# Performance work log

Measured on AMD Instinct MI355X. Metric: run time of the kernel, lower is better.

The kernel has to match this reference:

```python
import jax, jax.numpy as jnp
import numpy as np

DIM = 2048
N_HEADS = 16
HEAD_DIM = DIM // N_HEADS
GROUP_SIZE = 128
THRESHOLD = 0.5
EPS = 1e-8
B, T = 2, 2048


def _ternary_dequant(w):
    # groupwise absmean ternary quantize + dequant; DIM % GROUP_SIZE == 0 so no pad
    O, I = w.shape
    g = I // GROUP_SIZE
    wg = w.reshape(O, g, GROUP_SIZE)
    scale = jnp.clip(jnp.mean(jnp.abs(wg), axis=-1, keepdims=True), EPS)
    wn = wg / scale
    q = jnp.where(wn > THRESHOLD, 1.0, jnp.where(wn < -THRESHOLD, -1.0, 0.0))
    return (q * scale).reshape(O, I)


def _bitlinear(x, w):
    # STE: forward uses quantized weight
    w_ste = w + jax.lax.stop_gradient(_ternary_dequant(w) - w)
    return x @ w_ste.T


def _rope_tables(t, head_dim, base=10000.0):
    half = head_dim // 2
    inv_freq = 1.0 / (base ** (jnp.arange(half, dtype=jnp.float32) / half))
    freqs = jnp.outer(jnp.arange(t, dtype=jnp.float32), inv_freq)  # [T, half]
    return jnp.cos(freqs), jnp.sin(freqs)


def _apply_rope(x, cos, sin):
    # x: [B, H, T, D]
    d = x.shape[-1]
    x1, x2 = x[..., : d // 2], x[..., d // 2 :]
    cos = cos[None, None, :, :]
    sin = sin[None, None, :, :]
    return jnp.concatenate([x1 * cos - x2 * sin, x1 * sin + x2 * cos], axis=-1)


def setup_inputs() -> dict:
    key = jax.random.key(0)
    ks = jax.random.split(key, 5)
    std = 1.0 / np.sqrt(DIM)
    return {
        "x": jax.random.normal(ks[0], (B, T, DIM), dtype=jnp.float32),
        "w_q": jax.random.normal(ks[1], (DIM, DIM), dtype=jnp.float32) * std,
        "w_k": jax.random.normal(ks[2], (DIM, DIM), dtype=jnp.float32) * std,
        "w_v": jax.random.normal(ks[3], (DIM, DIM), dtype=jnp.float32) * std,
        "w_o": jax.random.normal(ks[4], (DIM, DIM), dtype=jnp.float32) * std,
    }


def reference(x, w_q, w_k, w_v, w_o):
    b, t, c = x.shape
    scale = HEAD_DIM ** -0.5

    def split_heads(y):
        return y.reshape(b, t, N_HEADS, HEAD_DIM).transpose(0, 2, 1, 3)  # [B,H,T,D]

    q = split_heads(_bitlinear(x, w_q))
    k = split_heads(_bitlinear(x, w_k))
    v = split_heads(_bitlinear(x, w_v))

    cos, sin = _rope_tables(t, HEAD_DIM)
    q = _apply_rope(q, cos, sin)
    k = _apply_rope(k, cos, sin)

    scores = jnp.einsum("bhqd,bhkd->bhqk", q, k) * scale
    causal = jnp.triu(jnp.ones((t, t), dtype=bool), k=1)
    scores = jnp.where(causal[None, None], -jnp.inf, scores)
    probs = jax.nn.softmax(scores, axis=-1)
    y = jnp.einsum("bhqk,bhkd->bhqd", probs, v)
    y = y.transpose(0, 2, 1, 3).reshape(b, t, c)
    return _bitlinear(y, w_o)
```

## Files before the change

kernel.cpp:

```cpp
#include <hip/hip_runtime.h>
#include <stdint.h>
#include <math.h>

#define DIMC 2048
#define NHEADS 16
#define HDIM 128
#define TSEQ 2048
#define NTOK 4096

using bf16x8 = __attribute__((ext_vector_type(8))) short;
using f32x4  = __attribute__((ext_vector_type(4))) float;

typedef __attribute__((address_space(1))) const void gas_void;
typedef __attribute__((address_space(3))) void las_void;

static __device__ __forceinline__ unsigned short f2b(float f) {
  union { float f; unsigned int u; } a; a.f = f;
  unsigned int u = a.u;
  u = (u + 0x7fffu + ((u >> 16) & 1u)) >> 16;
  return (unsigned short)u;
}
static __device__ __forceinline__ float b2f(unsigned short s) {
  union { unsigned int u; float f; } a; a.u = ((unsigned int)s) << 16;
  return a.f;
}

__global__ void detect_dtype(const unsigned short* __restrict__ xs,
                             int* __restrict__ flag)
{
  const int lane = threadIdx.x;
  const unsigned short u = xs[2 * lane];
  const int e = (u >> 7) & 0xFF;
  const bool plausible = (e >= 112) && (e <= 135);
  const unsigned long long m = __ballot(plausible);
  if (lane == 0) *flag = (__popcll(m) >= 32) ? 1 : 0;
}

static __device__ __forceinline__ void dequant_one(
    const void* __restrict__ w, unsigned short* __restrict__ o,
    int grp, int lane, int isbf16)
{
  float a, bq;
  if (isbf16) {
    const unsigned int pk =
        ((const unsigned int*)((const unsigned short*)w + (long)grp * 128))[lane];
    a  = b2f((unsigned short)(pk & 0xffffu));
    bq = b2f((unsigned short)(pk >> 16));
  } else {
    const float2 v = ((const float2*)((const float*)w + (long)grp * 128))[lane];
    a = v.x; bq = v.y;
  }
  double s = fabs((double)a) + fabs((double)bq);
  #pragma unroll
  for (int off = 1; off < 64; off <<= 1) s += __shfl_xor(s, off);
  double scale = s * (1.0 / 128.0);
  if (scale < 1e-8) scale = 1e-8;
  const float fs = (float)scale;
  const double wn0 = (double)a / scale;
  const double wn1 = (double)bq / scale;
  const float q0 = (wn0 > 0.5) ? fs : ((wn0 < -0.5) ? -fs : 0.0f);
  const float q1 = (wn1 > 0.5) ? fs : ((wn1 < -0.5) ? -fs : 0.0f);
  const unsigned int opk = (unsigned int)f2b(q0) | ((unsigned int)f2b(q1) << 16);
  ((unsigned int*)o)[(long)grp * 64 + lane] = opk;
}

__global__ void __launch_bounds__(256) dequant_auto(
    const void* __restrict__ w, unsigned short* __restrict__ o,
    const int* __restrict__ flag)
{
  const int wave = threadIdx.x >> 6, lane = threadIdx.x & 63;
  dequant_one(w, o, blockIdx.x * 4 + wave, lane, *flag);
}

__global__ void __launch_bounds__(256) dequant3(
    const void* __restrict__ w0, const void* __restrict__ w1,
    const void* __restrict__ w2, unsigned short* __restrict__ o,
    const int* __restrict__ flag)
{
  const int wave = threadIdx.x >> 6, lane = threadIdx.x & 63;
  const void* w = (blockIdx.y == 0) ? w0 : (blockIdx.y == 1) ? w1 : w2;
  unsigned short* oo = o + (long)blockIdx.y * DIMC * DIMC;
  dequant_one(w, oo, blockIdx.x * 4 + wave, lane, *flag);
}

__global__ void __launch_bounds__(256) cast_auto(
    const void* __restrict__ x, unsigned short* __restrict__ o,
    const int* __restrict__ flag)
{
  const int i = (blockIdx.x * 256 + threadIdx.x) * 4;
  if (*flag) {
    *(ushort4*)(o + i) = *(const ushort4*)((const unsigned short*)x + i);
  } else {
    const float4 v = *(const float4*)((const float*)x + i);
    ushort4 u;
    u.x = f2b(v.x); u.y = f2b(v.y); u.z = f2b(v.z); u.w = f2b(v.w);
    *(ushort4*)(o + i) = u;
  }
}

__device__ __forceinline__ void storeOne(float* C, long i, float v) { C[i] = v; }
__device__ __forceinline__ void storeOne(unsigned short* C, long i, float v) { C[i] = f2b(v); }

template <typename OUTT>
static __device__ __forceinline__ void gemm_tile(
    const unsigned short* __restrict__ A, const unsigned short* __restrict__ B,
    OUTT* __restrict__ C, int m0, int n0, int Nc, int K,
    unsigned short* As, unsigned short* Bs)
{
  const int tid = threadIdx.x;
  const int wave = tid >> 6;
  const int lane = tid & 63;
  const int wr = (wave >> 1) * 64, wc = (wave & 1) * 64;
  const int c16 = lane & 15, q4 = lane >> 4;

  f32x4 acc[4][4];
  #pragma unroll
  for (int i = 0; i < 4; i++)
    #pragma unroll
    for (int j = 0; j < 4; j++)
      acc[i][j] = (f32x4){0.f, 0.f, 0.f, 0.f};

  const int srow = tid >> 2;
  const int scol = (tid & 3) * 8;
  const unsigned short* ga = A + (long)(m0 + srow) * K + scol;
  const unsigned short* gb = B + (long)(n0 + srow) * K + scol;

  for (int k0 = 0; k0 < K; k0 += 64) {
    #pragma unroll
    for (int h = 0; h < 2; h++)
      #pragma unroll
      for (int i = 0; i < 2; i++) {
        __builtin_amdgcn_global_load_lds(
            (gas_void*)(ga + (long)i * 64 * K + k0 + h * 32),
            (las_void*)(As + h * 4096 + i * 2048 + wave * 512), 16, 0, 0);
        __builtin_amdgcn_global_load_lds(
            (gas_void*)(gb + (long)i * 64 * K + k0 + h * 32),
            (las_void*)(Bs + h * 4096 + i * 2048 + wave * 512), 16, 0, 0);
      }
    __syncthreads();
    #pragma unroll
    for (int kc = 0; kc < 2; kc++) {
      bf16x8 af[4], bfr[4];
      #pragma unroll
      for (int t = 0; t < 4; t++) {
        af[t]  = *(const bf16x8*)(As + kc * 4096 + (wr + t * 16 + c16) * 32 + q4 * 8);
        bfr[t] = *(const bf16x8*)(Bs + kc * 4096 + (wc + t * 16 + c16) * 32 + q4 * 8);
      }
      #pragma unroll
      for (int mt = 0; mt < 4; mt++)
        #pragma unroll
        for (int nt = 0; nt < 4; nt++)
          acc[mt][nt] = __builtin_amdgcn_mfma_f32_16x16x32_bf16(af[mt], bfr[nt], acc[mt][nt], 0, 0, 0);
    }
    __syncthreads();
  }

  #pragma unroll
  for (int mt = 0; mt < 4; mt++) {
    const int m = m0 + wr + mt * 16 + q4 * 4;
    #pragma unroll
    for (int nt = 0; nt < 4; nt++) {
      const int n = wc + nt * 16 + c16;
      #pragma unroll
      for (int r = 0; r < 4; r++)
        storeOne(C, (long)(m + r) * Nc + n, acc[mt][nt][r]);
    }
  }
}

template <typename OUTT>
__global__ void __launch_bounds__(256) gemm_bt(
    const unsigned short* __restrict__ A, const unsigned short* __restrict__ B,
    OUTT* __restrict__ C, int M, int N, int K)
{
  __shared__ unsigned short As[128 * 64];
  __shared__ unsigned short Bs[128 * 64];
  gemm_tile<OUTT>(A, B, C + blockIdx.x * 128, blockIdx.y * 128, blockIdx.x * 128,
                  N, K, As, Bs);
}

__global__ void __launch_bounds__(256) gemm_qkv(
    const unsigned short* __restrict__ A, const unsigned short* __restrict__ B,
    unsigned short* __restrict__ C0, unsigned short* __restrict__ C1,
    unsigned short* __restrict__ C2, int K)
{
  __shared__ unsigned short As[128 * 64];
  __shared__ unsigned short Bs[128 * 64];
  const int n0 = blockIdx.x * 128;
  unsigned short* Cb = (n0 < 2048) ? C0 : (n0 < 4096) ? C1 : C2;
  gemm_tile<unsigned short>(A, B, Cb + (n0 & 2047), blockIdx.y * 128, n0,
                            DIMC, K, As, Bs);
}

__global__ void __launch_bounds__(256) rope_kernel(
    unsigned short* __restrict__ Q, unsigned short* __restrict__ Kb)
{
  const int idx = blockIdx.x * 256 + threadIdx.x;
  const int d = idx & 63;
  const int h = (idx >> 6) & (NHEADS - 1);
  const int row = idx >> 10;
  const int t = row & (TSEQ - 1);
  const float inv_freq = expf(-9.210340371976184f * (float)d * (1.0f / 64.0f));
  float sn, cs;
  sincosf((float)t * inv_freq, &sn, &cs);
  const long base = (long)row * DIMC + h * HDIM + d;
  float x1 = b2f(Q[base]), x2 = b2f(Q[base + 64]);
  Q[base]      = f2b(x1 * cs - x2 * sn);
  Q[base + 64] = f2b(x1 * sn + x2 * cs);
  x1 = b2f(Kb[base]); x2 = b2f(Kb[base + 64]);
  Kb[base]      = f2b(x1 * cs - x2 * sn);
  Kb[base + 64] = f2b(x1 * sn + x2 * cs);
}

#define FA_M 16.0f
__global__ void __launch_bounds__(256) fattn(
    const unsigned short* __restrict__ Q,
    const unsigned short* __restrict__ K,
    const unsigned short* __restrict__ V,
    unsigned short* __restrict__ Y)
{
  __shared__ unsigned short SU[9216];
  __shared__ unsigned short VT[128 * 72];
  __shared__ float red[4][32];

  const int tid = threadIdx.x, wave = tid >> 6, lane = tid & 63;
  const int idx = blockIdx.x;
  const int qt = 15 - (idx >> 5);
  const int bh = idx & 31;
  const int b = bh >> 4, h = bh & 15;
  const int qbase = qt * 128;
  const int qw = wave * 32;
  const int c = lane & 15, g = lane >> 4;
  const long tokbase = (long)b * TSEQ;
  const int col0 = h * HDIM;

  bf16x8 qf[2][4];
  #pragma unroll
  for (int qq = 0; qq < 2; qq++) {
    const unsigned short* qp =
        Q + (tokbase + qbase + qw + qq * 16 + c) * DIMC + col0 + g * 8;
    #pragma unroll
    for (int kc = 0; kc < 4; kc++) qf[qq][kc] = *(const bf16x8*)(qp + kc * 32);
  }

  f32x4 od[8][2];
  #pragma unroll
  for (int dt = 0; dt < 8; dt++)
    #pragma unroll
    for (int qq = 0; qq < 2; qq++)
      od[dt][qq] = (f32x4){0.f, 0.f, 0.f, 0.f};
  float lpart[2][4];
  #pragma unroll
  for (int qq = 0; qq < 2; qq++)
    #pragma unroll
    for (int r = 0; r < 4; r++) lpart[qq][r] = 0.0f;

  const int ksr = tid >> 2, ksc = (tid & 3) * 32;
  const int vk0 = (tid & 31) * 2, vd0 = (tid >> 5) * 16;

  const float SC = 0.088388347648318447f;
  const int nkt = 2 * qt + 2;

  float4 kr0, kr1, kr2, kr3;
  bf16x8 va0, va1, vb0, vb1;
  {
    const unsigned short* src = K + (tokbase + ksr) * DIMC + col0 + ksc;
    kr0 = ((const float4*)src)[0]; kr1 = ((const float4*)src)[1];
    kr2 = ((const float4*)src)[2]; kr3 = ((const float4*)src)[3];
    const unsigned short* s0 = V + (tokbase + vk0) * DIMC + col0 + vd0;
    const unsigned short* s1 = s0 + DIMC;
    va0 = *(const bf16x8*)(s0); va1 = *(const bf16x8*)(s0 + 8);
    vb0 = *(const bf16x8*)(s1); vb1 = *(const bf16x8*)(s1 + 8);
  }

  for (int kt = 0; kt < nkt; kt++) {
    const int kb = kt * 64;
    __syncthreads();
    {
      float4* dst = (float4*)&SU[ksr * 136 + ksc];
      dst[0] = kr0; dst[1] = kr1; dst[2] = kr2; dst[3] = kr3;
    }
    {
      #pragma unroll
      for (int dd = 0; dd < 8; dd++) {
        const unsigned int p0 =
            (unsigned int)(unsigned short)va0[dd] |
            ((unsigned int)(unsigned short)vb0[dd] << 16);
        *(unsigned int*)&VT[(vd0 + dd) * 72 + vk0] = p0;
      }
      #pragma unroll
      for (int dd = 0; dd < 8; dd++) {
        const unsigned int p1 =
            (unsigned int)(unsigned short)va1[dd] |
            ((unsigned int)(unsigned short)vb1[dd] << 16);
        *(unsigned int*)&VT[(vd0 + 8 + dd) * 72 + vk0] = p1;
      }
    }
    __syncthreads();

    if (kt + 1 < nkt) {
      const int kb2 = kb + 64;
      const unsigned short* src = K + (tokbase + kb2 + ksr) * DIMC + col0 + ksc;
      kr0 = ((const float4*)src)[0]; kr1 = ((const float4*)src)[1];
      kr2 = ((const float4*)src)[2]; kr3 = ((const float4*)src)[3];
      const unsigned short* s0 = V + (tokbase + kb2 + vk0) * DIMC + col0 + vd0;
      const unsigned short* s1 = s0 + DIMC;
      va0 = *(const bf16x8*)(s0); va1 = *(const bf16x8*)(s0 + 8);
      vb0 = *(const bf16x8*)(s1); vb1 = *(const bf16x8*)(s1 + 8);
    }

    f32x4 sacc[2][4];
    #pragma unroll
    for (int qq = 0; qq < 2; qq++)
      #pragma unroll
      for (int nt = 0; nt < 4; nt++) sacc[qq][nt] = (f32x4){0.f, 0.f, 0.f, 0.f};
    #pragma unroll
    for (int kc = 0; kc < 4; kc++) {
      bf16x8 bk[4];
      #pragma unroll
      for (int nt = 0; nt < 4; nt++)
        bk[nt] = *(const bf16x8*)&SU[(nt * 16 + c) * 136 + kc * 32 + g * 8];
      #pragma unroll
      for (int qq = 0; qq < 2; qq++)
        #pragma unroll
        for (int nt = 0; nt < 4; nt++)
          sacc[qq][nt] = __builtin_amdgcn_mfma_f32_16x16x32_bf16(
              qf[qq][kc], bk[nt], sacc[qq][nt], 0, 0, 0);
    }
    __syncthreads();

    #pragma unroll
    for (int qq = 0; qq < 2; qq++)
      #pragma unroll
      for (int r = 0; r < 4; r++) {
        const int qg = qbase + qw + qq * 16 + g * 4 + r;
        #pragma unroll
        for (int nt = 0; nt < 4; nt++) {
          const int kg = kb + nt * 16 + c;
          const float sv = sacc[qq][nt][r] * SC - FA_M;
          const float p = (kg > qg) ? 0.0f : __expf(sv);
          lpart[qq][r] += p;
          SU[(wave * 32 + qq * 16 + g * 4 + r) * 72 + nt * 16 + c] = f2b(p);
        }
      }

    #pragma unroll
    for (int kc = 0; kc < 2; kc++) {
      bf16x8 pb[2];
      #pragma unroll
      for (int qq = 0; qq < 2; qq++)
        pb[qq] = *(const bf16x8*)&SU[(wave * 32 + qq * 16 + c) * 72 + kc * 32 + g * 8];
      #pragma unroll
      for (int dt = 0; dt < 8; dt++) {
        bf16x8 va = *(const bf16x8*)&VT[(dt * 16 + c) * 72 + kc * 32 + g * 8];
        #pragma unroll
        for (int qq = 0; qq < 2; qq++)
          od[dt][qq] = __builtin_amdgcn_mfma_f32_16x16x32_bf16(
              va, pb[qq], od[dt][qq], 0, 0, 0);
      }
    }
  }

  #pragma unroll
  for (int qq = 0; qq < 2; qq++)
    #pragma unroll
    for (int r = 0; r < 4; r++) {
      float l = lpart[qq][r];
      #pragma unroll
      for (int off = 1; off < 16; off <<= 1) l += __shfl_xor(l, off);
      lpart[qq][r] = l;
    }
  __syncthreads();
  if (c == 0) {
    #pragma unroll
    for (int qq = 0; qq < 2; qq++)
      #pragma unroll
      for (int r = 0; r < 4; r++)
        red[wave][qq * 16 + g * 4 + r] = 1.0f / lpart[qq][r];
  }
  __syncthreads();
  #pragma unroll
  for (int qq = 0; qq < 2; qq++) {
    const float linv = red[wave][qq * 16 + c];
    unsigned short* yp =
        Y + (tokbase + qbase + qw + qq * 16 + c) * DIMC + col0;
    #pragma unroll
    for (int dt = 0; dt < 8; dt++)
      #pragma unroll
      for (int r = 0; r < 4; r++)
        yp[dt * 16 + g * 4 + r] = f2b(od[dt][qq][r] * linv);
  }
}

extern "C" void kernel_launch(void* const* d_in, const int* in_sizes, int n_in,
                              void* d_out, int out_size, void* d_ws, size_t ws_size,
                              hipStream_t stream)
{
  const void* x  = d_in[0];
  const void* wq = d_in[1];
  const void* wk = d_in[2];
  const void* wv = d_in[3];
  const void* wo = d_in[4];
  float* out = (float*)d_out;

  char* ws = (char*)d_ws;
  const size_t MB = 1024 * 1024;
  unsigned short* wbuf = (unsigned short*)(ws + 0 * MB);
  unsigned short* xb   = (unsigned short*)(ws + 24 * MB);
  unsigned short* Qb   = (unsigned short*)(ws + 40 * MB);
  unsigned short* Kb   = (unsigned short*)(ws + 56 * MB);
  unsigned short* Vb   = (unsigned short*)(ws + 72 * MB);
  int* flag            = (int*)(ws + 88 * MB);
  unsigned short* Yb   = xb;

  detect_dtype<<<dim3(1), 64, 0, stream>>>((const unsigned short*)x, flag);
  cast_auto<<<dim3(8192), 256, 0, stream>>>(x, xb, flag);
  dequant3<<<dim3(8192, 3), 256, 0, stream>>>(wq, wk, wv, wbuf, flag);
  gemm_qkv<<<dim3(48, 32), 256, 0, stream>>>(xb, wbuf, Qb, Kb, Vb, DIMC);
  rope_kernel<<<dim3(16384), 256, 0, stream>>>(Qb, Kb);
  fattn<<<dim3(512), 256, 0, stream>>>(Qb, Kb, Vb, Yb);
  dequant_auto<<<dim3(8192), 256, 0, stream>>>(wo, wbuf, flag);
  gemm_bt<float><<<dim3(16, 32), 256, 0, stream>>>(Yb, wbuf, out, NTOK, DIMC, DIMC);
}
```

Baseline: 408.2 us.

## Fuse RoPE into QKV GEMM epilogue and reorder attention tile schedule

The GEMM tile's N-columns are remapped so each wave holds both rotary halves (d and d+64) of a head in registers. RoPE can then be applied in the QKV GEMM epilogue for the Q and K tiles, and the separate rope kernel with its extra read/write pass over Q and K is removed. The attention block-to-query-tile mapping also changes so the second half of blocks runs short tiles in ascending order, pairing heavy and light causal tiles. Using fast __cosf/__sinf with fp32 values before bf16 rounding slightly changes numerics.

```diff
diff --git a/kernel.cpp b/kernel.cpp
--- a/kernel.cpp
+++ b/kernel.cpp
@@ -101,7 +101,7 @@
 __device__ __forceinline__ void storeOne(float* C, long i, float v) { C[i] = v; }
 __device__ __forceinline__ void storeOne(unsigned short* C, long i, float v) { C[i] = f2b(v); }
 
-template <typename OUTT>
+template <typename OUTT, bool ROPE>
 static __device__ __forceinline__ void gemm_tile(
     const unsigned short* __restrict__ A, const unsigned short* __restrict__ B,
     OUTT* __restrict__ C, int m0, int n0, int Nc, int K,
@@ -110,7 +110,8 @@
   const int tid = threadIdx.x;
   const int wave = tid >> 6;
   const int lane = tid & 63;
-  const int wr = (wave >> 1) * 64, wc = (wave & 1) * 64;
+  const int wr = (wave >> 1) * 64;
+  const int wc2 = (wave & 1) * 32;
   const int c16 = lane & 15, q4 = lane >> 4;
 
   f32x4 acc[4][4];
@@ -143,8 +144,9 @@
       bf16x8 af[4], bfr[4];
       #pragma unroll
       for (int t = 0; t < 4; t++) {
+        const int nrow = wc2 + (t & 1) * 16 + (t >> 1) * 64 + c16;
         af[t]  = *(const bf16x8*)(As + kc * 4096 + (wr + t * 16 + c16) * 32 + q4 * 8);
-        bfr[t] = *(const bf16x8*)(Bs + kc * 4096 + (wc + t * 16 + c16) * 32 + q4 * 8);
+        bfr[t] = *(const bf16x8*)(Bs + kc * 4096 + nrow * 32 + q4 * 8);
       }
       #pragma unroll
       for (int mt = 0; mt < 4; mt++)
@@ -155,12 +157,34 @@
     __syncthreads();
   }
 
+  if (ROPE) {
+    float invf[2];
+    #pragma unroll
+    for (int j2 = 0; j2 < 2; j2++)
+      invf[j2] = __expf(-0.14391565f * (float)(wc2 + j2 * 16 + c16));
+    #pragma unroll
+    for (int mt = 0; mt < 4; mt++)
+      #pragma unroll
+      for (int r = 0; r < 4; r++) {
+        const int m = m0 + wr + mt * 16 + q4 * 4 + r;
+        const float t = (float)(m & (TSEQ - 1));
+        #pragma unroll
+        for (int j2 = 0; j2 < 2; j2++) {
+          const float ang = t * invf[j2];
+          const float cs = __cosf(ang), sn = __sinf(ang);
+          const float x1 = acc[mt][j2][r], x2 = acc[mt][j2 + 2][r];
+          acc[mt][j2][r]     = x1 * cs - x2 * sn;
+          acc[mt][j2 + 2][r] = x1 * sn + x2 * cs;
+        }
+      }
+  }
+
   #pragma unroll
   for (int mt = 0; mt < 4; mt++) {
     const int m = m0 + wr + mt * 16 + q4 * 4;
     #pragma unroll
     for (int nt = 0; nt < 4; nt++) {
-      const int n = wc + nt * 16 + c16;
+      const int n = wc2 + (nt & 1) * 16 + (nt >> 1) * 64 + c16;
       #pragma unroll
       for (int r = 0; r < 4; r++)
         storeOne(C, (long)(m + r) * Nc + n, acc[mt][nt][r]);
@@ -175,8 +199,8 @@
 {
   __shared__ unsigned short As[128 * 64];
   __shared__ unsigned short Bs[128 * 64];
-  gemm_tile<OUTT>(A, B, C + blockIdx.x * 128, blockIdx.y * 128, blockIdx.x * 128,
-                  N, K, As, Bs);
+  gemm_tile<OUTT, false>(A, B, C + blockIdx.x * 128, blockIdx.y * 128,
+                         blockIdx.x * 128, N, K, As, Bs);
 }
 
 __global__ void __launch_bounds__(256) gemm_qkv(
@@ -188,28 +212,12 @@
   __shared__ unsigned short Bs[128 * 64];
   const int n0 = blockIdx.x * 128;
   unsigned short* Cb = (n0 < 2048) ? C0 : (n0 < 4096) ? C1 : C2;
-  gemm_tile<unsigned short>(A, B, Cb + (n0 & 2047), blockIdx.y * 128, n0,
-                            DIMC, K, As, Bs);
-}
-
-__global__ void __launch_bounds__(256) rope_kernel(
-    unsigned short* __restrict__ Q, unsigned short* __restrict__ Kb)
-{
-  const int idx = blockIdx.x * 256 + threadIdx.x;
-  const int d = idx & 63;
-  const int h = (idx >> 6) & (NHEADS - 1);
-  const int row = idx >> 10;
-  const int t = row & (TSEQ - 1);
-  const float inv_freq = expf(-9.210340371976184f * (float)d * (1.0f / 64.0f));
-  float sn, cs;
-  sincosf((float)t * inv_freq, &sn, &cs);
-  const long base = (long)row * DIMC + h * HDIM + d;
-  float x1 = b2f(Q[base]), x2 = b2f(Q[base + 64]);
-  Q[base]      = f2b(x1 * cs - x2 * sn);
-  Q[base + 64] = f2b(x1 * sn + x2 * cs);
-  x1 = b2f(Kb[base]); x2 = b2f(Kb[base + 64]);
-  Kb[base]      = f2b(x1 * cs - x2 * sn);
-  Kb[base + 64] = f2b(x1 * sn + x2 * cs);
+  if (n0 < 4096)
+    gemm_tile<unsigned short, true>(A, B, Cb + (n0 & 2047), blockIdx.y * 128,
+                                    n0, DIMC, K, As, Bs);
+  else
+    gemm_tile<unsigned short, false>(A, B, Cb + (n0 & 2047), blockIdx.y * 128,
+                                     n0, DIMC, K, As, Bs);
 }
 
 #define FA_M 16.0f
@@ -225,7 +233,7 @@
 
   const int tid = threadIdx.x, wave = tid >> 6, lane = tid & 63;
   const int idx = blockIdx.x;
-  const int qt = 15 - (idx >> 5);
+  const int qt = (idx < 256) ? (15 - (idx >> 5)) : ((idx - 256) >> 5);
   const int bh = idx & 31;
   const int b = bh >> 4, h = bh & 15;
   const int qbase = qt * 128;
@@ -417,7 +425,6 @@
   cast_auto<<<dim3(8192), 256, 0, stream>>>(x, xb, flag);
   dequant3<<<dim3(8192, 3), 256, 0, stream>>>(wq, wk, wv, wbuf, flag);
   gemm_qkv<<<dim3(48, 32), 256, 0, stream>>>(xb, wbuf, Qb, Kb, Vb, DIMC);
-  rope_kernel<<<dim3(16384), 256, 0, stream>>>(Qb, Kb);
   fattn<<<dim3(512), 256, 0, stream>>>(Qb, Kb, Vb, Yb);
   dequant_auto<<<dim3(8192), 256, 0, stream>>>(wo, wbuf, flag);
   gemm_bt<float><<<dim3(16, 32), 256, 0, stream>>>(Yb, wbuf, out, NTOK, DIMC, DIMC);
```

Result: slower. 427.7 us (+4.8%).
